# Kernel optimization log

Measured on AMD Instinct MI355X. Metric: run time of the kernel, lower is better.

The kernel has to match this reference:

```python
import jax, jax.numpy as jnp
import numpy as np

N_HEAD = 16
D_MODEL = 1024
# c_attn compression metadata (coeff_ratio=0.25, 'medium')
ATTN_N = D_MODEL * 3 * D_MODEL          # 3145728
ATTN_PAD = 4194304                       # next pow2
ATTN_FFT = ATTN_PAD // 2 + 1             # 2097153
ATTN_KEEP = int(ATTN_FFT * 0.25)         # 524288
PROJ_N = D_MODEL * D_MODEL               # 1048576 (already pow2)
PROJ_PAD = PROJ_N
PROJ_FFT = PROJ_PAD // 2 + 1             # 524289
PROJ_KEEP = int(PROJ_FFT * 0.25)         # 131072


def setup_inputs() -> dict:
    key = jax.random.key(0)
    ks = jax.random.split(key, 9)
    B, S = 2, 2048
    x = jax.random.normal(ks[0], (B, S, D_MODEL), dtype=jnp.float32)
    c_attn_re = jax.random.normal(ks[1], (ATTN_KEEP,), dtype=jnp.float32)
    c_attn_im = jax.random.normal(ks[2], (ATTN_KEEP,), dtype=jnp.float32)
    # indices from topk are unique -> use a random permutation prefix
    c_attn_idx = jax.random.permutation(ks[3], ATTN_FFT)[:ATTN_KEEP].astype(jnp.int32)
    c_attn_scale = jnp.ones((1,), dtype=jnp.float32)
    c_proj_re = jax.random.normal(ks[4], (PROJ_KEEP,), dtype=jnp.float32)
    c_proj_im = jax.random.normal(ks[5], (PROJ_KEEP,), dtype=jnp.float32)
    c_proj_idx = jax.random.permutation(ks[6], PROJ_FFT)[:PROJ_KEEP].astype(jnp.int32)
    c_proj_scale = jnp.ones((1,), dtype=jnp.float32)
    c_attn_bias = jax.random.normal(ks[7], (3 * D_MODEL,), dtype=jnp.float32)
    c_proj_bias = jax.random.normal(ks[8], (D_MODEL,), dtype=jnp.float32)
    return dict(x=x, c_attn_re=c_attn_re, c_attn_im=c_attn_im, c_attn_idx=c_attn_idx,
                c_attn_scale=c_attn_scale, c_proj_re=c_proj_re, c_proj_im=c_proj_im,
                c_proj_idx=c_proj_idx, c_proj_scale=c_proj_scale,
                c_attn_bias=c_attn_bias, c_proj_bias=c_proj_bias)


def _decompress(re, im, idx, fft_len, pad_n, n, shape, scale):
    # zero-init + scatter of kept complex coeffs, then inverse rFFT
    full = jnp.zeros((fft_len,), dtype=jnp.complex64).at[idx].set(re + 1j * im)
    restored = jnp.fft.irfft(full, n=pad_n)[:n]
    return restored.reshape(shape) * scale[0]


def reference(x, c_attn_re, c_attn_im, c_attn_idx, c_attn_scale,
              c_proj_re, c_proj_im, c_proj_idx, c_proj_scale,
              c_attn_bias, c_proj_bias):
    Wa = _decompress(c_attn_re, c_attn_im, c_attn_idx, ATTN_FFT, ATTN_PAD,
                     ATTN_N, (D_MODEL, 3 * D_MODEL), c_attn_scale)
    Wp = _decompress(c_proj_re, c_proj_im, c_proj_idx, PROJ_FFT, PROJ_PAD,
                     PROJ_N, (D_MODEL, D_MODEL), c_proj_scale)
    B, S, _ = x.shape
    hd = D_MODEL // N_HEAD
    # F.linear(x, W.T, b) == x @ W + b  (Conv1D convention)
    qkv = x @ Wa + c_attn_bias                       # [B,S,3D]
    q, k, v = jnp.split(qkv, 3, axis=2)
    def heads(t):  # [B,S,D] -> [B,H,S,hd]
        return t.reshape(B, S, N_HEAD, hd).transpose(0, 2, 1, 3)
    q, k, v = heads(q), heads(k), heads(v)
    scores = jnp.einsum('bhqd,bhkd->bhqk', q, k) / jnp.sqrt(jnp.float32(hd))
    attn = jax.nn.softmax(scores, axis=-1)           # dropout = identity (eval)
    out = jnp.einsum('bhqk,bhkd->bhqd', attn, v)
    out = out.transpose(0, 2, 1, 3).reshape(B, S, D_MODEL)
    return out @ Wp + c_proj_bias
```

## Files before the change

### kernel.cpp

```cpp
#include <hip/hip_runtime.h>
#include <math.h>

#define N_HEADC  16
#define D_MODELC 1024
#define ATTN_N_C    3145728
#define ATTN_PAD_C  4194304
#define ATTN_NC     2097152
#define ATTN_KEEP_C 524288
#define PROJ_N_C    1048576
#define PROJ_PAD_C  1048576
#define PROJ_NC     524288
#define PROJ_KEEP_C 131072
#define BATCH_C 2
#define SEQ_C   2048

#define CEXP_C 0.18033688011112042f

typedef __attribute__((ext_vector_type(8))) short s16x8;
typedef __attribute__((ext_vector_type(4))) float f32x4;

#define AS1U(p) ((const __attribute__((address_space(1))) uint*)(p))
#define AS3U(p) ((__attribute__((address_space(3))) uint*)(p))

static __device__ __forceinline__ ushort f2bf(float f) {
    __bf16 b = (__bf16)f;
    return __builtin_bit_cast(ushort, b);
}
static __device__ __forceinline__ float bf2f(ushort u) {
    return __builtin_bit_cast(float, ((uint)u) << 16);
}
static __device__ __forceinline__ float2 cmul(float2 a, float2 b) {
    return make_float2(a.x * b.x - a.y * b.y, a.x * b.y + a.y * b.x);
}
static __device__ __forceinline__ float2 cadd(float2 a, float2 b) {
    return make_float2(a.x + b.x, a.y + b.y);
}
static __device__ __forceinline__ float2 csub(float2 a, float2 b) {
    return make_float2(a.x - b.x, a.y - b.y);
}
static __device__ __forceinline__ float2 crot(float2 z) {
    return make_float2(-z.y, z.x);
}

static __device__ __forceinline__ void r8core(const float2* a, float2* B) {
    const float2 t0 = cadd(a[0], a[4]), t1 = csub(a[0], a[4]);
    const float2 t2 = cadd(a[2], a[6]), t3 = csub(a[2], a[6]);
    const float2 t4 = cadd(a[1], a[5]), t5 = csub(a[1], a[5]);
    const float2 t6 = cadd(a[3], a[7]), t7 = csub(a[3], a[7]);
    const float2 E0 = cadd(t0, t2), E2 = csub(t0, t2);
    const float2 E1 = cadd(t1, crot(t3)), E3 = csub(t1, crot(t3));
    const float2 F0 = cadd(t4, t6), F2 = csub(t4, t6);
    const float2 F1 = cadd(t5, crot(t7)), F3 = csub(t5, crot(t7));
    const float c = 0.70710678118654752f;
    const float2 G1 = make_float2(c * (F1.x - F1.y), c * (F1.x + F1.y));
    const float2 G2 = crot(F2);
    const float2 G3 = make_float2(c * (-F3.x - F3.y), c * (F3.x - F3.y));
    B[0] = cadd(E0, F0); B[4] = csub(E0, F0);
    B[1] = cadd(E1, G1); B[5] = csub(E1, G1);
    B[2] = cadd(E2, G2); B[6] = csub(E2, G2);
    B[3] = cadd(E3, G3); B[7] = csub(E3, G3);
}

__global__ void scatter_half2(
    const float* __restrict__ re_a, const float* __restrict__ im_a,
    const int* __restrict__ idx_a, float2* __restrict__ Ha,
    const float* __restrict__ re_p, const float* __restrict__ im_p,
    const int* __restrict__ idx_p, float2* __restrict__ Hp) {
    int t = blockIdx.x * blockDim.x + threadIdx.x;
    if (t < ATTN_KEEP_C) {
        Ha[idx_a[t]] = make_float2(re_a[t], im_a[t]);
    } else {
        int u = t - ATTN_KEEP_C;
        Hp[idx_p[u]] = make_float2(re_p[u], im_p[u]);
    }
}

__global__ void pack_z(const float2* __restrict__ H, float2* __restrict__ Z,
                       int Nc, float th0) {
    int k = blockIdx.x * blockDim.x + threadIdx.x;
    if (k >= Nc) return;
    float2 g = H[k];
    float2 hm = H[Nc - k];
    if (k == 0) { g.y = 0.f; hm.y = 0.f; }
    float2 gh = make_float2(hm.x, -hm.y);
    float2 sum = make_float2(g.x + gh.x, g.y + gh.y);
    float2 dif = make_float2(g.x - gh.x, g.y - gh.y);
    float si, co;
    __sincosf(th0 * (float)k, &si, &co);
    float2 t = make_float2(dif.x * co - dif.y * si, dif.x * si + dif.y * co);
    Z[k] = make_float2(sum.x - t.y, sum.y + t.x);
}

__global__ void fft_stage(const float2* __restrict__ in, float2* __restrict__ out,
                          int slog, int m, int half) {
    int t = blockIdx.x * blockDim.x + threadIdx.x;
    if (t >= half) return;
    int s = 1 << slog;
    int q = t & (s - 1);
    int p = t >> slog;
    float si, co;
    __sincosf((float)(M_PI / (double)m) * (float)p, &si, &co);
    float2 a = in[q + s * p];
    float2 b = in[q + s * (p + m)];
    float2 su = cadd(a, b);
    float2 di = csub(a, b);
    int ob = q + ((s << 1) * p);
    out[ob]     = su;
    out[ob + s] = make_float2(di.x * co - di.y * si, di.x * si + di.y * co);
}

__global__ void fft_stage_r8(const float2* __restrict__ in, float2* __restrict__ out,
                             int slog, int M, float ang0, int eighth) {
    int t = blockIdx.x * blockDim.x + threadIdx.x;
    if (t >= eighth) return;
    const int s = 1 << slog;
    const int q = t & (s - 1);
    const int p = t >> slog;
    float2 a[8];
#pragma unroll
    for (int j = 0; j < 8; ++j)
        a[j] = in[q + (size_t)s * (p + j * M)];
    float2 B[8];
    r8core(a, B);
    float si, co;
    __sincosf(ang0 * (float)p, &si, &co);
    const float2 w = make_float2(co, si);
    const int ob = q + 8 * s * p;
    out[ob] = B[0];
    float2 wj = w;
    out[ob + s] = cmul(wj, B[1]);
#pragma unroll
    for (int j = 2; j < 8; ++j) {
        wj = cmul(wj, w);
        out[ob + j * s] = cmul(wj, B[j]);
    }
}

__global__ __launch_bounds__(256) void fft_stage_r64(
    const float2* __restrict__ in, float2* __restrict__ out, int slog, int M) {
    __shared__ float2 Ysh[32][8][9];
    const int tid = threadIdx.x;
    const int g = tid & 31, u = tid >> 5;
    const int s = 1 << slog;
    const int M8 = M >> 3;
    const int G = blockIdx.x * 32 + g;
    const int q = G & (s - 1);
    const int p0 = G >> slog;

    const int p = p0 + u * M8;
    float2 a[8];
#pragma unroll
    for (int j = 0; j < 8; ++j)
        a[j] = in[q + (size_t)s * (p + j * M)];
    float2 B[8];
    r8core(a, B);
    float si, co;
    __sincosf((0.78539816339744831f / (float)M) * (float)p, &si, &co);
    const float2 w = make_float2(co, si);
    Ysh[g][u][0] = B[0];
    float2 wj = w;
    Ysh[g][u][1] = cmul(wj, B[1]);
#pragma unroll
    for (int j = 2; j < 8; ++j) {
        wj = cmul(wj, w);
        Ysh[g][u][j] = cmul(wj, B[j]);
    }
    __syncthreads();

    float2 z[8];
#pragma unroll
    for (int jp = 0; jp < 8; ++jp)
        z[jp] = Ysh[g][jp][u];
    float2 B2[8];
    r8core(z, B2);
    __sincosf((0.78539816339744831f / (float)M8) * (float)p0, &si, &co);
    const float2 w2 = make_float2(co, si);
    const size_t ob = (size_t)q + (size_t)u * s + (size_t)64 * s * p0;
    out[ob] = B2[0];
    float2 wj2 = w2;
    out[ob + (size_t)8 * s] = cmul(wj2, B2[1]);
#pragma unroll
    for (int j2 = 2; j2 < 8; ++j2) {
        wj2 = cmul(wj2, w2);
        out[ob + (size_t)j2 * 8 * s] = cmul(wj2, B2[j2]);
    }
}

__global__ __launch_bounds__(256) void transpose_wz_bf16(
    const float2* __restrict__ z, ushort* __restrict__ WT,
    int Kd, int Nd, float inv, const float* __restrict__ sc, int qcols) {
    __shared__ float T[32][33];
    const int n0 = blockIdx.x * 32, k0 = blockIdx.y * 32;
    const int tx = threadIdx.x & 31, ty = threadIdx.x >> 5;
    const float s = inv * sc[0];
    for (int r = ty; r < 32; r += 8) {
        size_t j = (size_t)(k0 + r) * Nd + n0 + tx;
        float2 zz = z[j >> 1];
        T[r][tx] = (j & 1) ? zz.y : zz.x;
    }
    __syncthreads();
    for (int r = ty; r < 32; r += 8) {
        const float fs = ((n0 + r) < qcols) ? s * CEXP_C : s;
        WT[(size_t)(n0 + r) * Kd + k0 + tx] = f2bf(T[tx][r] * fs);
    }
}

__global__ void x_to_bf16(const float* __restrict__ x, ushort* __restrict__ xb, int n4) {
    int i = blockIdx.x * blockDim.x + threadIdx.x;
    if (i >= n4) return;
    float4 v = *(const float4*)(x + (size_t)i * 4);
    ushort4 o;
    o.x = f2bf(v.x); o.y = f2bf(v.y); o.z = f2bf(v.z); o.w = f2bf(v.w);
    *(ushort4*)(xb + (size_t)i * 4) = o;
}

template <int OUTMODE>
__global__ __launch_bounds__(256) void gemm_bt_mfma(
    const ushort* __restrict__ A, const ushort* __restrict__ Bt,
    const float* __restrict__ bias, void* __restrict__ Cout,
    ushort* __restrict__ Vt, int M, int N, int K, int NBX) {
    __shared__ ushort As[128 * 64];
    __shared__ ushort Bs[128 * 64];
    const int L = blockIdx.x;
    const int rsw = (L & 7) * ((int)gridDim.x >> 3) + (L >> 3);
    const int bx = rsw % NBX, by = rsw / NBX;
    const int tid = threadIdx.x;
    const int wid = tid >> 6, lane = tid & 63, quad = lane >> 4, l16 = lane & 15;
    const int row0 = by * 128, col0 = bx * 128;
    const int mh = (wid >> 1) * 64, nh = (wid & 1) * 64;
    const int r7 = l16 & 7;

    f32x4 acc[4][4] = {};

    for (int k0 = 0; k0 < K; k0 += 64) {
        __syncthreads();
#pragma unroll
        for (int rep = 0; rep < 4; ++rep) {
            int c = tid + rep * 256;
            int r = c >> 3;
            int kc = (c & 7) ^ (r & 7);
            ushort* lbA = &As[(rep * 256 + wid * 64) * 8];
            ushort* lbB = &Bs[(rep * 256 + wid * 64) * 8];
            __builtin_amdgcn_global_load_lds(
                AS1U(A + (size_t)(row0 + r) * K + k0 + kc * 8), AS3U(lbA), 16, 0, 0);
            __builtin_amdgcn_global_load_lds(
                AS1U(Bt + (size_t)(col0 + r) * K + k0 + kc * 8), AS3U(lbB), 16, 0, 0);
        }
        __syncthreads();
#pragma unroll
        for (int kk = 0; kk < 2; ++kk) {
            const int slot = ((kk * 4 + quad) ^ r7) * 8;
            s16x8 af[4], bfr[4];
#pragma unroll
            for (int mi = 0; mi < 4; ++mi)
                af[mi] = *(const s16x8*)&As[(mh + mi * 16 + l16) * 64 + slot];
#pragma unroll
            for (int ni = 0; ni < 4; ++ni)
                bfr[ni] = *(const s16x8*)&Bs[(nh + ni * 16 + l16) * 64 + slot];
#pragma unroll
            for (int mi = 0; mi < 4; ++mi)
#pragma unroll
                for (int ni = 0; ni < 4; ++ni)
                    acc[mi][ni] = __builtin_amdgcn_mfma_f32_16x16x32_bf16(
                        af[mi], bfr[ni], acc[mi][ni], 0, 0, 0);
        }
    }

#pragma unroll
    for (int mi = 0; mi < 4; ++mi)
#pragma unroll
        for (int ni = 0; ni < 4; ++ni) {
            const int col = col0 + nh + ni * 16 + l16;
            const int rbase = row0 + mh + mi * 16 + quad * 4;
            float bv = bias[col];
            if (OUTMODE == 1 && col < 1024) bv *= CEXP_C;
            if (OUTMODE == 0) {
                float* C = (float*)Cout;
#pragma unroll
                for (int j = 0; j < 4; ++j)
                    C[(size_t)(rbase + j) * N + col] = acc[mi][ni][j] + bv;
            } else {
                if (col < 2048) {
                    ushort* C = (ushort*)Cout;
#pragma unroll
                    for (int j = 0; j < 4; ++j)
                        C[(size_t)(rbase + j) * N + col] = f2bf(acc[mi][ni][j] + bv);
                } else {
                    const int bb = rbase >> 11;
                    const int seq = rbase & 2047;
                    const int d = col - 2048;
                    ushort4 pk;
                    pk.x = f2bf(acc[mi][ni][0] + bv);
                    pk.y = f2bf(acc[mi][ni][1] + bv);
                    pk.z = f2bf(acc[mi][ni][2] + bv);
                    pk.w = f2bf(acc[mi][ni][3] + bv);
                    *(ushort4*)&Vt[(size_t)bb * 2097152 + (size_t)d * 2048 + seq] = pk;
                }
            }
        }
}

__global__ __launch_bounds__(256, 4) void attn_fwd_mfma(
    const ushort* __restrict__ qkv, const ushort* __restrict__ Vt,
    ushort* __restrict__ Op, float* __restrict__ Lp) {
    const int L = blockIdx.x;
    const int xcd = L & 7, slot = L >> 3;
    const int g = xcd * 4 + (slot >> 5);
    const int within = slot & 31;
    const int b = g >> 4, h = g & 15;
    const int qb = within >> 1, split = within & 1;
    const int tid = threadIdx.x;
    const int wid = tid >> 6, lane = tid & 63, quad = lane >> 4, l16 = lane & 15;
    const int wq = wid * 32;
    const int kt0 = split * 16;
    const int r7 = l16 & 7;

    __shared__ ushort Ks[64 * 64];
    __shared__ ushort Vts[64 * 64];
    __shared__ ushort Ps[128 * 64];

#pragma unroll
    for (int rep = 0; rep < 4; ++rep) {
        int c = tid + rep * 256;
        int r = c >> 3;
        int kc = (c & 7) ^ (r & 7);
        ushort* lb = &Ps[(rep * 256 + wid * 64) * 8];
        __builtin_amdgcn_global_load_lds(
            AS1U(qkv + (size_t)(b * 2048 + qb * 128 + r) * 3072 + h * 64 + kc * 8),
            AS3U(lb), 16, 0, 0);
    }
    __syncthreads();

    s16x8 qreg[2][2];
#pragma unroll
    for (int ks = 0; ks < 2; ++ks) {
        const int slot2 = ((ks * 4 + quad) ^ r7) * 8;
#pragma unroll
        for (int ni = 0; ni < 2; ++ni)
            qreg[ks][ni] = *(const s16x8*)&Ps[(wq + ni * 16 + l16) * 64 + slot2];
    }

    f32x4 o[4][2] = {};
    float l_r[2] = {0.f, 0.f};

    for (int tt = 0; tt < 16; ++tt) {
        __syncthreads();
        const int kt = kt0 + tt;
#pragma unroll
        for (int rep = 0; rep < 2; ++rep) {
            int c = tid + rep * 256;
            int r = c >> 3;
            int kc = (c & 7) ^ (r & 7);
            ushort* lbK = &Ks[(rep * 256 + wid * 64) * 8];
            ushort* lbV = &Vts[(rep * 256 + wid * 64) * 8];
            __builtin_amdgcn_global_load_lds(
                AS1U(qkv + (size_t)(b * 2048 + kt * 64 + r) * 3072 + 1024 + h * 64 + kc * 8),
                AS3U(lbK), 16, 0, 0);
            __builtin_amdgcn_global_load_lds(
                AS1U(Vt + (size_t)b * 2097152 + (size_t)(h * 64 + r) * 2048 + kt * 64 + kc * 8),
                AS3U(lbV), 16, 0, 0);
        }
        __syncthreads();

        f32x4 s[4][2] = {};
#pragma unroll
        for (int ks = 0; ks < 2; ++ks) {
            const int slot2 = ((ks * 4 + quad) ^ r7) * 8;
            s16x8 ka[4];
#pragma unroll
            for (int mi = 0; mi < 4; ++mi)
                ka[mi] = *(const s16x8*)&Ks[(mi * 16 + l16) * 64 + slot2];
#pragma unroll
            for (int mi = 0; mi < 4; ++mi)
#pragma unroll
                for (int ni = 0; ni < 2; ++ni)
                    s[mi][ni] = __builtin_amdgcn_mfma_f32_16x16x32_bf16(
                        ka[mi], qreg[ks][ni], s[mi][ni], 0, 0, 0);
        }

#pragma unroll
        for (int ni = 0; ni < 2; ++ni)
#pragma unroll
            for (int mi = 0; mi < 4; ++mi) {
                ushort4 pk;
#pragma unroll
                for (int j = 0; j < 4; ++j) {
                    float p = exp2f(s[mi][ni][j]);
                    l_r[ni] += p;
                    ((ushort*)&pk)[j] = f2bf(p);
                }
                const int jq = 2 * mi + (quad >> 1);
                *(ushort4*)&Ps[(wq + ni * 16 + l16) * 64 + ((jq ^ r7)) * 8 + (quad & 1) * 4] = pk;
            }

#pragma unroll
        for (int ks = 0; ks < 2; ++ks) {
            const int slot2 = ((ks * 4 + quad) ^ r7) * 8;
            s16x8 va[4], pb[2];
#pragma unroll
            for (int md = 0; md < 4; ++md)
                va[md] = *(const s16x8*)&Vts[(md * 16 + l16) * 64 + slot2];
#pragma unroll
            for (int ni = 0; ni < 2; ++ni)
                pb[ni] = *(const s16x8*)&Ps[(wq + ni * 16 + l16) * 64 + slot2];
#pragma unroll
            for (int md = 0; md < 4; ++md)
#pragma unroll
                for (int ni = 0; ni < 2; ++ni)
                    o[md][ni] = __builtin_amdgcn_mfma_f32_16x16x32_bf16(
                        va[md], pb[ni], o[md][ni], 0, 0, 0);
        }
    }

#pragma unroll
    for (int ni = 0; ni < 2; ++ni) {
        float l = l_r[ni];
        l += __shfl_xor(l, 16);
        l += __shfl_xor(l, 32);
        const size_t row = (size_t)(b * 2048 + qb * 128 + wq + ni * 16 + l16);
        if (quad == 0)
            Lp[(size_t)split * 65536 + row * 16 + h] = l;
#pragma unroll
        for (int md = 0; md < 4; ++md) {
            ushort4 pk;
#pragma unroll
            for (int j = 0; j < 4; ++j)
                ((ushort*)&pk)[j] = f2bf(o[md][ni][j]);
            *(ushort4*)&Op[(size_t)split * 4194304 + row * 1024 + h * 64 + md * 16 + quad * 4] = pk;
        }
    }
}

__global__ __launch_bounds__(256) void attn_reduce(
    const ushort* __restrict__ Op, const float* __restrict__ Lp,
    ushort* __restrict__ ctx) {
    const int i = blockIdx.x * 256 + threadIdx.x;
    const size_t base = (size_t)i * 4;
    const int row = (int)(base >> 10);
    const int hh = (int)((base & 1023) >> 6);
    const float l = Lp[row * 16 + hh] + Lp[65536 + row * 16 + hh];
    const float inv = 1.f / l;
    ushort4 a = *(const ushort4*)&Op[base];
    ushort4 b = *(const ushort4*)&Op[4194304 + base];
    ushort4 o;
    o.x = f2bf((bf2f(a.x) + bf2f(b.x)) * inv);
    o.y = f2bf((bf2f(a.y) + bf2f(b.y)) * inv);
    o.z = f2bf((bf2f(a.z) + bf2f(b.z)) * inv);
    o.w = f2bf((bf2f(a.w) + bf2f(b.w)) * inv);
    *(ushort4*)&ctx[base] = o;
}

extern "C" void kernel_launch(void* const* d_in, const int* in_sizes, int n_in,
                              void* d_out, int out_size, void* d_ws, size_t ws_size,
                              hipStream_t stream) {
    const float* x        = (const float*)d_in[0];
    const float* attn_re  = (const float*)d_in[1];
    const float* attn_im  = (const float*)d_in[2];
    const int*   attn_idx = (const int*)d_in[3];
    const float* attn_sc  = (const float*)d_in[4];
    const float* proj_re  = (const float*)d_in[5];
    const float* proj_im  = (const float*)d_in[6];
    const int*   proj_idx = (const int*)d_in[7];
    const float* proj_sc  = (const float*)d_in[8];
    const float* attn_b   = (const float*)d_in[9];
    const float* proj_b   = (const float*)d_in[10];
    float* out = (float*)d_out;

    const size_t MB = 1048576;
    char* w = (char*)d_ws;
    float2* A0  = (float2*)(w);
    float2* A1  = (float2*)(w + 16 * MB);
    float2* Ha  = (float2*)(w + 32 * MB);
    float2* Hp  = (float2*)(w + 49 * MB);
    float2* P0  = (float2*)(w + 54 * MB);
    float2* P1  = (float2*)(w + 58 * MB);
    ushort* WaT = (ushort*)(w + 62 * MB);
    ushort* WpT = (ushort*)(w + 68 * MB);
    ushort* x_bf= (ushort*)(w + 70 * MB);
    ushort* qkvb= (ushort*)(w);
    ushort* Vt  = (ushort*)(w + 24 * MB);
    ushort* ctx = (ushort*)(w + 32 * MB);
    ushort* Op  = (ushort*)(w + 40 * MB);
    float*  Lp  = (float*)(w + 56 * MB);

    x_to_bf16<<<4096, 256, 0, stream>>>(x, x_bf, 1048576);

    hipMemsetAsync(w + 32 * MB, 0, 22 * MB, stream);
    scatter_half2<<<(ATTN_KEEP_C + PROJ_KEEP_C) / 256, 256, 0, stream>>>(
        attn_re, attn_im, attn_idx, Ha, proj_re, proj_im, proj_idx, Hp);

    pack_z<<<ATTN_NC / 256, 256, 0, stream>>>(Ha, A0, ATTN_NC, (float)(2.0 * M_PI / ATTN_PAD_C));
    fft_stage_r64<<<(ATTN_NC / 8) / 256, 256, 0, stream>>>(A0, A1, 0,  ATTN_NC >> 3);
    fft_stage_r64<<<(ATTN_NC / 8) / 256, 256, 0, stream>>>(A1, A0, 6,  ATTN_NC >> 9);
    fft_stage_r64<<<(ATTN_NC / 8) / 256, 256, 0, stream>>>(A0, A1, 12, ATTN_NC >> 15);
    fft_stage_r8 <<<(ATTN_NC / 8) / 256, 256, 0, stream>>>(A1, A0, 18, 1,
        (float)(M_PI / 4.0), ATTN_NC / 8);
    transpose_wz_bf16<<<dim3(3072 / 32, 1024 / 32), 256, 0, stream>>>(
        A0, WaT, 1024, 3072, 1.f / ATTN_PAD_C, attn_sc, 1024);

    pack_z<<<PROJ_NC / 256, 256, 0, stream>>>(Hp, P0, PROJ_NC, (float)(2.0 * M_PI / PROJ_PAD_C));
    fft_stage<<<(PROJ_NC / 2) / 256, 256, 0, stream>>>(P0, P1, 0, PROJ_NC / 2, PROJ_NC / 2);
    fft_stage_r64<<<(PROJ_NC / 8) / 256, 256, 0, stream>>>(P1, P0, 1,  PROJ_NC >> 4);
    fft_stage_r64<<<(PROJ_NC / 8) / 256, 256, 0, stream>>>(P0, P1, 7,  PROJ_NC >> 10);
    fft_stage_r64<<<(PROJ_NC / 8) / 256, 256, 0, stream>>>(P1, P0, 13, PROJ_NC >> 16);
    transpose_wz_bf16<<<dim3(1024 / 32, 1024 / 32), 256, 0, stream>>>(
        P0, WpT, 1024, 1024, 1.f / PROJ_PAD_C, proj_sc, 0);

    gemm_bt_mfma<1><<<768, 256, 0, stream>>>(
        x_bf, WaT, attn_b, qkvb, Vt, 4096, 3072, 1024, 24);

    attn_fwd_mfma<<<1024, 256, 0, stream>>>(qkvb, Vt, Op, Lp);
    attn_reduce<<<4096, 256, 0, stream>>>(Op, Lp, ctx);

    gemm_bt_mfma<0><<<256, 256, 0, stream>>>(
        ctx, WpT, proj_b, out, (ushort*)nullptr, 4096, 1024, 1024, 8);
}
```

Baseline: 299.9 us.

## Batch attn and proj FFT stages into shared dual-role kernel launches

Merges the independent attention-weight and projection-weight decompression pipelines into combined launches. Block index picks which problem each block works on, so the scatter, pack, FFT stages and transpose each run as one launch, and x conversion is folded into the scatter kernel. This cuts the kernel count from about 16 to 7 and lets the small proj work fill idle CUs. It also drops the swizzled block-to-tile mapping in the GEMM in favour of a plain 2D grid, which may reduce L2 locality.

```diff
diff --git a/kernel.cpp b/kernel.cpp
--- a/kernel.cpp
+++ b/kernel.cpp
@@ -61,23 +61,11 @@
     B[3] = cadd(E3, G3); B[7] = csub(E3, G3);
 }
 
-__global__ void scatter_half2(
-    const float* __restrict__ re_a, const float* __restrict__ im_a,
-    const int* __restrict__ idx_a, float2* __restrict__ Ha,
-    const float* __restrict__ re_p, const float* __restrict__ im_p,
-    const int* __restrict__ idx_p, float2* __restrict__ Hp) {
-    int t = blockIdx.x * blockDim.x + threadIdx.x;
-    if (t < ATTN_KEEP_C) {
-        Ha[idx_a[t]] = make_float2(re_a[t], im_a[t]);
-    } else {
-        int u = t - ATTN_KEEP_C;
-        Hp[idx_p[u]] = make_float2(re_p[u], im_p[u]);
-    }
-}
-
-__global__ void pack_z(const float2* __restrict__ H, float2* __restrict__ Z,
-                       int Nc, float th0) {
-    int k = blockIdx.x * blockDim.x + threadIdx.x;
+
+
+static __device__ __forceinline__ void pack_body(
+    const float2* __restrict__ H, float2* __restrict__ Z,
+    int Nc, float th0, int k) {
     if (k >= Nc) return;
     float2 g = H[k];
     float2 hm = H[Nc - k];
@@ -91,9 +79,9 @@
     Z[k] = make_float2(sum.x - t.y, sum.y + t.x);
 }
 
-__global__ void fft_stage(const float2* __restrict__ in, float2* __restrict__ out,
-                          int slog, int m, int half) {
-    int t = blockIdx.x * blockDim.x + threadIdx.x;
+static __device__ __forceinline__ void r2_body(
+    const float2* __restrict__ in, float2* __restrict__ out,
+    int slog, int m, int half, int t) {
     if (t >= half) return;
     int s = 1 << slog;
     int q = t & (s - 1);
@@ -109,9 +97,9 @@
     out[ob + s] = make_float2(di.x * co - di.y * si, di.x * si + di.y * co);
 }
 
-__global__ void fft_stage_r8(const float2* __restrict__ in, float2* __restrict__ out,
-                             int slog, int M, float ang0, int eighth) {
-    int t = blockIdx.x * blockDim.x + threadIdx.x;
+static __device__ __forceinline__ void r8_body(
+    const float2* __restrict__ in, float2* __restrict__ out,
+    int slog, int M, float ang0, int eighth, int t) {
     if (t >= eighth) return;
     const int s = 1 << slog;
     const int q = t & (s - 1);
@@ -136,14 +124,15 @@
     }
 }
 
-__global__ __launch_bounds__(256) void fft_stage_r64(
-    const float2* __restrict__ in, float2* __restrict__ out, int slog, int M) {
-    __shared__ float2 Ysh[32][8][9];
+static __device__ void r64_body(
+    float2 (*Ysh)[8][9],
+    const float2* __restrict__ in, float2* __restrict__ out,
+    int slog, int M, int vb) {
     const int tid = threadIdx.x;
     const int g = tid & 31, u = tid >> 5;
     const int s = 1 << slog;
     const int M8 = M >> 3;
-    const int G = blockIdx.x * 32 + g;
+    const int G = vb * 32 + g;
     const int q = G & (s - 1);
     const int p0 = G >> slog;
 
@@ -186,11 +175,11 @@
     }
 }
 
-__global__ __launch_bounds__(256) void transpose_wz_bf16(
-    const float2* __restrict__ z, ushort* __restrict__ WT,
-    int Kd, int Nd, float inv, const float* __restrict__ sc, int qcols) {
-    __shared__ float T[32][33];
-    const int n0 = blockIdx.x * 32, k0 = blockIdx.y * 32;
+static __device__ __forceinline__ void transpose_body(
+    float (*T)[33], const float2* __restrict__ z, ushort* __restrict__ WT,
+    int Kd, int Nd, float inv, const float* __restrict__ sc, int qcols, int vb) {
+    const int nbx = Nd >> 5;
+    const int n0 = (vb % nbx) * 32, k0 = (vb / nbx) * 32;
     const int tx = threadIdx.x & 31, ty = threadIdx.x >> 5;
     const float s = inv * sc[0];
     for (int r = ty; r < 32; r += 8) {
@@ -205,28 +194,92 @@
     }
 }
 
-__global__ void x_to_bf16(const float* __restrict__ x, ushort* __restrict__ xb, int n4) {
-    int i = blockIdx.x * blockDim.x + threadIdx.x;
-    if (i >= n4) return;
-    float4 v = *(const float4*)(x + (size_t)i * 4);
-    ushort4 o;
-    o.x = f2bf(v.x); o.y = f2bf(v.y); o.z = f2bf(v.z); o.w = f2bf(v.w);
-    *(ushort4*)(xb + (size_t)i * 4) = o;
+
+__global__ __launch_bounds__(256) void x_scatter(
+    const float* __restrict__ x, ushort* __restrict__ xb,
+    const float* __restrict__ re_a, const float* __restrict__ im_a,
+    const int* __restrict__ idx_a, float2* __restrict__ Ha,
+    const float* __restrict__ re_p, const float* __restrict__ im_p,
+    const int* __restrict__ idx_p, float2* __restrict__ Hp) {
+    const int B = blockIdx.x;
+    if (B < 4096) {
+        const int i = B * 256 + threadIdx.x;
+        float4 v = *(const float4*)(x + (size_t)i * 4);
+        ushort4 o;
+        o.x = f2bf(v.x); o.y = f2bf(v.y); o.z = f2bf(v.z); o.w = f2bf(v.w);
+        *(ushort4*)(xb + (size_t)i * 4) = o;
+    } else {
+        const int t = (B - 4096) * 256 + threadIdx.x;
+        if (t < ATTN_KEEP_C) {
+            Ha[idx_a[t]] = make_float2(re_a[t], im_a[t]);
+        } else {
+            const int u = t - ATTN_KEEP_C;
+            Hp[idx_p[u]] = make_float2(re_p[u], im_p[u]);
+        }
+    }
+}
+
+__global__ __launch_bounds__(256) void pack_dual(
+    const float2* __restrict__ Ha, float2* __restrict__ Za, float tha,
+    const float2* __restrict__ Hp, float2* __restrict__ Zp, float thp) {
+    const int B = blockIdx.x;
+    if (B < 8192)
+        pack_body(Ha, Za, ATTN_NC, tha, B * 256 + (int)threadIdx.x);
+    else
+        pack_body(Hp, Zp, PROJ_NC, thp, (B - 8192) * 256 + (int)threadIdx.x);
+}
+
+__global__ __launch_bounds__(256) void fft_r64_r2(
+    const float2* __restrict__ ia, float2* __restrict__ oa, int sla, int Ma, int na,
+    const float2* __restrict__ ip, float2* __restrict__ op, int mp, int halfp) {
+    __shared__ float2 Ysh[32][8][9];
+    if ((int)blockIdx.x < na)
+        r64_body(Ysh, ia, oa, sla, Ma, blockIdx.x);
+    else
+        r2_body(ip, op, 0, mp, halfp, (blockIdx.x - na) * 256 + threadIdx.x);
+}
+
+__global__ __launch_bounds__(256) void fft_r64_dual(
+    const float2* __restrict__ ia, float2* __restrict__ oa, int sla, int Ma, int na,
+    const float2* __restrict__ ip, float2* __restrict__ op, int slp, int Mp) {
+    __shared__ float2 Ysh[32][8][9];
+    if ((int)blockIdx.x < na)
+        r64_body(Ysh, ia, oa, sla, Ma, blockIdx.x);
+    else
+        r64_body(Ysh, ip, op, slp, Mp, blockIdx.x - na);
+}
+
+__global__ __launch_bounds__(256) void fft_r8_r64(
+    const float2* __restrict__ ia, float2* __restrict__ oa, int sla, float ang0,
+    int eighth, int na,
+    const float2* __restrict__ ip, float2* __restrict__ op, int slp, int Mp) {
+    __shared__ float2 Ysh[32][8][9];
+    if ((int)blockIdx.x < na)
+        r8_body(ia, oa, sla, 1, ang0, eighth, (blockIdx.x) * 256 + threadIdx.x);
+    else
+        r64_body(Ysh, ip, op, slp, Mp, blockIdx.x - na);
+}
+
+__global__ __launch_bounds__(256) void transpose_dual(
+    const float2* __restrict__ za, ushort* __restrict__ Wa, const float* __restrict__ sca,
+    const float2* __restrict__ zp, ushort* __restrict__ Wp, const float* __restrict__ scp) {
+    __shared__ float T[32][33];
+    if (blockIdx.x < 3072)
+        transpose_body(T, za, Wa, 1024, 3072, 1.f / ATTN_PAD_C, sca, 1024, blockIdx.x);
+    else
+        transpose_body(T, zp, Wp, 1024, 1024, 1.f / PROJ_PAD_C, scp, 0, blockIdx.x - 3072);
 }
 
 template <int OUTMODE>
 __global__ __launch_bounds__(256) void gemm_bt_mfma(
     const ushort* __restrict__ A, const ushort* __restrict__ Bt,
     const float* __restrict__ bias, void* __restrict__ Cout,
-    ushort* __restrict__ Vt, int M, int N, int K, int NBX) {
+    ushort* __restrict__ Vt, int M, int N, int K) {
     __shared__ ushort As[128 * 64];
     __shared__ ushort Bs[128 * 64];
-    const int L = blockIdx.x;
-    const int rsw = (L & 7) * ((int)gridDim.x >> 3) + (L >> 3);
-    const int bx = rsw % NBX, by = rsw / NBX;
     const int tid = threadIdx.x;
     const int wid = tid >> 6, lane = tid & 63, quad = lane >> 4, l16 = lane & 15;
-    const int row0 = by * 128, col0 = bx * 128;
+    const int row0 = blockIdx.y * 128, col0 = blockIdx.x * 128;
     const int mh = (wid >> 1) * 64, nh = (wid & 1) * 64;
     const int r7 = l16 & 7;
 
@@ -483,35 +536,32 @@
     ushort* Op  = (ushort*)(w + 40 * MB);
     float*  Lp  = (float*)(w + 56 * MB);
 
-    x_to_bf16<<<4096, 256, 0, stream>>>(x, x_bf, 1048576);
-
     hipMemsetAsync(w + 32 * MB, 0, 22 * MB, stream);
-    scatter_half2<<<(ATTN_KEEP_C + PROJ_KEEP_C) / 256, 256, 0, stream>>>(
-        attn_re, attn_im, attn_idx, Ha, proj_re, proj_im, proj_idx, Hp);
-
-    pack_z<<<ATTN_NC / 256, 256, 0, stream>>>(Ha, A0, ATTN_NC, (float)(2.0 * M_PI / ATTN_PAD_C));
-    fft_stage_r64<<<(ATTN_NC / 8) / 256, 256, 0, stream>>>(A0, A1, 0,  ATTN_NC >> 3);
-    fft_stage_r64<<<(ATTN_NC / 8) / 256, 256, 0, stream>>>(A1, A0, 6,  ATTN_NC >> 9);
-    fft_stage_r64<<<(ATTN_NC / 8) / 256, 256, 0, stream>>>(A0, A1, 12, ATTN_NC >> 15);
-    fft_stage_r8 <<<(ATTN_NC / 8) / 256, 256, 0, stream>>>(A1, A0, 18, 1,
-        (float)(M_PI / 4.0), ATTN_NC / 8);
-    transpose_wz_bf16<<<dim3(3072 / 32, 1024 / 32), 256, 0, stream>>>(
-        A0, WaT, 1024, 3072, 1.f / ATTN_PAD_C, attn_sc, 1024);
-
-    pack_z<<<PROJ_NC / 256, 256, 0, stream>>>(Hp, P0, PROJ_NC, (float)(2.0 * M_PI / PROJ_PAD_C));
-    fft_stage<<<(PROJ_NC / 2) / 256, 256, 0, stream>>>(P0, P1, 0, PROJ_NC / 2, PROJ_NC / 2);
-    fft_stage_r64<<<(PROJ_NC / 8) / 256, 256, 0, stream>>>(P1, P0, 1,  PROJ_NC >> 4);
-    fft_stage_r64<<<(PROJ_NC / 8) / 256, 256, 0, stream>>>(P0, P1, 7,  PROJ_NC >> 10);
-    fft_stage_r64<<<(PROJ_NC / 8) / 256, 256, 0, stream>>>(P1, P0, 13, PROJ_NC >> 16);
-    transpose_wz_bf16<<<dim3(1024 / 32, 1024 / 32), 256, 0, stream>>>(
-        P0, WpT, 1024, 1024, 1.f / PROJ_PAD_C, proj_sc, 0);
-
-    gemm_bt_mfma<1><<<768, 256, 0, stream>>>(
-        x_bf, WaT, attn_b, qkvb, Vt, 4096, 3072, 1024, 24);
+
+    x_scatter<<<6656, 256, 0, stream>>>(
+        x, x_bf, attn_re, attn_im, attn_idx, Ha, proj_re, proj_im, proj_idx, Hp);
+
+    pack_dual<<<10240, 256, 0, stream>>>(
+        Ha, A0, (float)(2.0 * M_PI / ATTN_PAD_C),
+        Hp, P0, (float)(2.0 * M_PI / PROJ_PAD_C));
+
+    fft_r64_r2 <<<2048, 256, 0, stream>>>(A0, A1, 0,  ATTN_NC >> 3,  1024,
+                                          P0, P1, PROJ_NC / 2, PROJ_NC / 2);
+    fft_r64_dual<<<1280, 256, 0, stream>>>(A1, A0, 6,  ATTN_NC >> 9,  1024,
+                                           P1, P0, 1,  PROJ_NC >> 4);
+    fft_r64_dual<<<1280, 256, 0, stream>>>(A0, A1, 12, ATTN_NC >> 15, 1024,
+                                           P0, P1, 7,  PROJ_NC >> 10);
+    fft_r8_r64 <<<1280, 256, 0, stream>>>(A1, A0, 18, (float)(M_PI / 4.0),
+                                          ATTN_NC / 8, 1024,
+                                          P1, P0, 13, PROJ_NC >> 16);
+    transpose_dual<<<4096, 256, 0, stream>>>(A0, WaT, attn_sc, P0, WpT, proj_sc);
+
+    gemm_bt_mfma<1><<<dim3(3072 / 128, 4096 / 128), 256, 0, stream>>>(
+        x_bf, WaT, attn_b, qkvb, Vt, 4096, 3072, 1024);
 
     attn_fwd_mfma<<<1024, 256, 0, stream>>>(qkvb, Vt, Op, Lp);
     attn_reduce<<<4096, 256, 0, stream>>>(Op, Lp, ctx);
 
-    gemm_bt_mfma<0><<<256, 256, 0, stream>>>(
-        ctx, WpT, proj_b, out, (ushort*)nullptr, 4096, 1024, 1024, 8);
-}
+    gemm_bt_mfma<0><<<dim3(1024 / 128, 4096 / 128), 256, 0, stream>>>(
+        ctx, WpT, proj_b, out, (ushort*)nullptr, 4096, 1024, 1024);
+}
```

Measured after the change: 275.1 us. 1.09x faster.
